# Optimization experiments

Measured on AMD Instinct MI355X. Metric: run time of the kernel, lower is better.

Reference implementation:

```python
import jax, jax.numpy as jnp
import numpy as np


def setup_inputs() -> dict:
    key = jax.random.key(0)
    k1, k2 = jax.random.split(key)
    K, D = 512, 64
    x = jax.random.normal(k1, (64, D, 32, 32), dtype=jnp.float32)
    # torch init: uniform(-1/k, 1/k)
    weight = jax.random.uniform(k2, (D, K), dtype=jnp.float32, minval=-1.0 / K, maxval=1.0 / K)
    return {"x": x, "weight": weight}


def reference(x, weight):
    # x: [B, d, *spatial]; weight: [d, k]
    B, d = x.shape[0], x.shape[1]
    spatial = x.shape[2:]
    xf = x.reshape(B, d, -1)                      # [B, d, N]
    x2 = jnp.sum(xf * xf, axis=1)                 # [B, N]
    w2 = jnp.sum(weight * weight, axis=0)         # [k]
    dots = jnp.einsum('bdn,dk->bnk', xf, weight)  # [B, N, k]
    dist = x2[..., None] - 2.0 * dots + w2        # [B, N, k]
    argmin = jnp.argmin(dist, axis=-1)            # [B, N]
    quantized = jnp.take(weight.T, argmin, axis=0)          # [B, N, d]
    quantized = jnp.moveaxis(quantized.reshape(B, *spatial, d), -1, 1)  # [B, d, *spatial]
    return quantized, argmin.reshape(B, *spatial)
```

## Files before the change

kernel.cpp:

```cpp
#include <hip/hip_runtime.h>

#define KCODES 512
#define DDIM   64
#define NPIX   1024
#define QELEMS (64 * DDIM * NPIX)
#define FLAG_GAP 8e-5f

typedef float f32x4 __attribute__((ext_vector_type(4)));
typedef short bf16x8 __attribute__((ext_vector_type(8)));
typedef unsigned int u32;
typedef u32 u32x4 __attribute__((ext_vector_type(4)));


__device__ __forceinline__ bf16x8 pack_hi(const float* f) {
  u32x4 wds;
#pragma unroll
  for (int p = 0; p < 4; ++p) {
    u32 u0 = __float_as_uint(f[2 * p]);
    u32 u1 = __float_as_uint(f[2 * p + 1]);
    wds[p] = (u0 >> 16) | (u1 & 0xffff0000u);
  }
  return __builtin_bit_cast(bf16x8, wds);
}
__device__ __forceinline__ bf16x8 pack_lo(const float* f) {
  u32x4 wds;
#pragma unroll
  for (int p = 0; p < 4; ++p) {
    float r0 = f[2 * p]     - __uint_as_float(__float_as_uint(f[2 * p])     & 0xffff0000u);
    float r1 = f[2 * p + 1] - __uint_as_float(__float_as_uint(f[2 * p + 1]) & 0xffff0000u);
    wds[p] = (__float_as_uint(r0) >> 16) | (__float_as_uint(r1) & 0xffff0000u);
  }
  return __builtin_bit_cast(bf16x8, wds);
}

__global__ void vq_prep(const float* __restrict__ w,
                        float* __restrict__ w2f_g,
                        bf16x8* __restrict__ frag) {
#pragma clang fp contract(off)
  const int blk = blockIdx.x;
  if (blk == 32) {
    int k = threadIdx.x;
    if (k < KCODES) {
      float s = 0.0f;
      for (int d = 0; d < DDIM; ++d) {
        float v = w[d * KCODES + k];
        float p = v * v;
        s = s + p;
      }
      w2f_g[k] = s;
    }
    return;
  }
  if (threadIdx.x >= 256) return;
  const int cg   = blk;
  const int t    = threadIdx.x >> 6;
  const int lane = threadIdx.x & 63;
  const int code = cg * 16 + (lane & 15);
  const int h    = t & 1;
  float f[8];
#pragma unroll
  for (int j = 0; j < 8; ++j)
    f[j] = w[(h * 32 + (lane >> 4) * 8 + j) * KCODES + code];
  frag[(cg * 4 + t) * 64 + lane] = (t < 2) ? pack_hi(f) : pack_lo(f);
}

__global__ __launch_bounds__(256) void vq_kernel(
    const float* __restrict__ x, const float* __restrict__ w,
    const float* __restrict__ w2f_g, const bf16x8* __restrict__ frag,
    float* __restrict__ qout, float* __restrict__ aout) {
#pragma clang fp contract(off)

  __shared__ float  xs[DDIM][65];
  __shared__ float  sx2[64];
  __shared__ float  w2fs[KCODES];
  __shared__ float  sm1[4][64], sm2[4][64];
  __shared__ int    si1[4][64];
  __shared__ int    skm[64];
  __shared__ unsigned long long s_fmask;

  const int tid  = threadIdx.x;
  const int lane = tid & 63;
  const int lr   = lane & 15;
  const int lg   = lane >> 4;
  const int wid  = __builtin_amdgcn_readfirstlane(tid >> 6);
  const int b    = blockIdx.x >> 4;
  const int n0   = (blockIdx.x & 15) << 6;
  const size_t pixbase = (size_t)blockIdx.x << 6;

  {
    const float* xp = x + (size_t)b * (DDIM * NPIX) + n0;
#pragma unroll
    for (int dd = 0; dd < 16; ++dd) {
      int d = dd * 4 + wid;
      xs[d][lane] = xp[(size_t)d * NPIX + lane];
    }
  }
  w2fs[tid]       = w2f_g[tid];
  w2fs[tid + 256] = w2f_g[tid + 256];
  __syncthreads();

  {
    float x2 = 0.0f;
#pragma unroll
    for (int d = 0; d < DDIM; ++d) {
      float xv = xs[d][lane];
      float p = xv * xv;
      x2 = x2 + p;
    }
    if (tid < 64) sx2[lane] = x2;
  }

  bf16x8 bxh[4][2], bxl[4][2];
#pragma unroll
  for (int pg = 0; pg < 4; ++pg) {
#pragma unroll
    for (int h = 0; h < 2; ++h) {
      float f[8];
#pragma unroll
      for (int j = 0; j < 8; ++j)
        f[j] = xs[h * 32 + lg * 8 + j][pg * 16 + lr];
      bxh[pg][h] = pack_hi(f);
      bxl[pg][h] = pack_lo(f);
    }
  }

  float m1a[4], m2a[4];
  int   i1a[4];
#pragma unroll
  for (int pg = 0; pg < 4; ++pg) { m1a[pg] = 3.4e38f; m2a[pg] = 3.4e38f; i1a[pg] = 0; }

#pragma unroll
  for (int cg = 0; cg < 8; ++cg) {
    const int codebase = wid * 128 + cg * 16;
    const bf16x8* fr = frag + (size_t)(wid * 8 + cg) * 4 * 64 + lane;
    bf16x8 awh0 = fr[0];
    bf16x8 awh1 = fr[64];
    bf16x8 awl0 = fr[128];
    bf16x8 awl1 = fr[192];

#pragma unroll
    for (int pg = 0; pg < 4; ++pg) {
      f32x4 acc = {0.f, 0.f, 0.f, 0.f};
      acc = __builtin_amdgcn_mfma_f32_16x16x32_bf16(awh0, bxh[pg][0], acc, 0, 0, 0);
      acc = __builtin_amdgcn_mfma_f32_16x16x32_bf16(awh1, bxh[pg][1], acc, 0, 0, 0);
      acc = __builtin_amdgcn_mfma_f32_16x16x32_bf16(awl0, bxh[pg][0], acc, 0, 0, 0);
      acc = __builtin_amdgcn_mfma_f32_16x16x32_bf16(awl1, bxh[pg][1], acc, 0, 0, 0);
      acc = __builtin_amdgcn_mfma_f32_16x16x32_bf16(awh0, bxl[pg][0], acc, 0, 0, 0);
      acc = __builtin_amdgcn_mfma_f32_16x16x32_bf16(awh1, bxl[pg][1], acc, 0, 0, 0);
      acc = __builtin_amdgcn_mfma_f32_16x16x32_bf16(awl0, bxl[pg][0], acc, 0, 0, 0);
      acc = __builtin_amdgcn_mfma_f32_16x16x32_bf16(awl1, bxl[pg][1], acc, 0, 0, 0);
#pragma unroll
      for (int r = 0; r < 4; ++r) {
        int code = codebase + lg * 4 + r;
        float s = w2fs[code] - 2.0f * acc[r];
        bool lt = s < m1a[pg];
        float om1 = m1a[pg];
        m2a[pg] = lt ? om1 : fminf(s, m2a[pg]);
        m1a[pg] = lt ? s : m1a[pg];
        i1a[pg] = lt ? code : i1a[pg];
      }
    }
  }

#pragma unroll
  for (int pg = 0; pg < 4; ++pg) {
#pragma unroll
    for (int mi = 0; mi < 2; ++mi) {
      int mask = mi ? 32 : 16;
      float pm1 = __shfl_xor(m1a[pg], mask);
      float pm2 = __shfl_xor(m2a[pg], mask);
      int   pi1 = __shfl_xor(i1a[pg], mask);
      if (pm1 < m1a[pg]) { m2a[pg] = fminf(m1a[pg], pm2); m1a[pg] = pm1; i1a[pg] = pi1; }
      else               { m2a[pg] = fminf(m2a[pg], pm1); }
    }
  }
  if (lg == 0) {
#pragma unroll
    for (int pg = 0; pg < 4; ++pg) {
      sm1[wid][pg * 16 + lr] = m1a[pg];
      sm2[wid][pg * 16 + lr] = m2a[pg];
      si1[wid][pg * 16 + lr] = i1a[pg];
    }
  }
  __syncthreads();

  if (tid < 64) {
    float M1 = sm1[0][lane], M2 = sm2[0][lane];
    int   I1 = si1[0][lane];
#pragma unroll
    for (int c = 1; c < 4; ++c) {
      float c1 = sm1[c][lane];
      if (c1 < M1) { M2 = fminf(M1, sm2[c][lane]); M1 = c1; I1 = si1[c][lane]; }
      else         { M2 = fminf(M2, c1); }
    }
    skm[lane] = I1;
    unsigned long long bal = __ballot(M2 - M1 < FLAG_GAP);
    if (lane == 0) s_fmask = bal;
  }
  __syncthreads();

  {
    unsigned long long fm = s_fmask;
    int idx = 0;
    while (fm) {
      const int L = __builtin_ctzll(fm);
      fm &= (fm - 1);
      if ((idx++ & 3) != wid) continue;
      const float x2L = sx2[L];
      const int k0 = lane * 8;
      float dots[8];
#pragma unroll
      for (int c = 0; c < 8; ++c) dots[c] = 0.f;
      for (int d = 0; d < DDIM; ++d) {
        float xv = xs[d][L];
        const float* wr = w + d * KCODES + k0;
#pragma unroll
        for (int c = 0; c < 8; ++c) {
          float p = xv * wr[c];
          dots[c] = dots[c] + p;
        }
      }
      float bv = 3.4e38f;
      int   bi = 0;
#pragma unroll
      for (int c = 0; c < 8; ++c) {
        float t  = x2L - 2.0f * dots[c];
        float s2 = t + w2fs[k0 + c];
        if (s2 < bv) { bv = s2; bi = k0 + c; }
      }
#pragma unroll
      for (int off = 1; off < 64; off <<= 1) {
        float ov = __shfl_xor(bv, off);
        int   oi = __shfl_xor(bi, off);
        if (ov < bv || (ov == bv && oi < bi)) { bv = ov; bi = oi; }
      }
      if (lane == 0) skm[L] = bi;
    }
  }
  __syncthreads();

  if (tid < 64) aout[pixbase + lane] = (float)skm[lane];

  const int kmin = skm[lane];
  float* qp = qout + (size_t)b * (DDIM * NPIX) + n0 + lane;
#pragma unroll
  for (int dd = 0; dd < 16; ++dd) {
    int d = wid * 16 + dd;
    qp[(size_t)d * NPIX] = w[d * KCODES + kmin];
  }
}

extern "C" void kernel_launch(void* const* d_in, const int* in_sizes, int n_in,
                              void* d_out, int out_size, void* d_ws, size_t ws_size,
                              hipStream_t stream) {
  const float* x = (const float*)d_in[0];
  const float* w = (const float*)d_in[1];
  float* qout = (float*)d_out;
  float* aout = (float*)d_out + QELEMS;

  char*   wsb   = (char*)d_ws;
  float*  w2f_g = (float*)wsb;
  bf16x8* frag  = (bf16x8*)(wsb + 4096);

  vq_prep<<<33, 512, 0, stream>>>(w, w2f_g, frag);
  vq_kernel<<<64 * 16, 256, 0, stream>>>(x, w, w2f_g, frag, qout, aout);
}
```

Baseline: 48.62 us.

## Halve pixels per block, vectorize fp32 fallback loads, tighten flag gap

Each block now handles 32 pixels instead of 64, which doubles the grid to 2048 blocks so more of the GPU is busy. The x tile load and quantized output store are rewritten as flat 256-thread loops over the smaller tile. The exact fp32 recheck loop now reads codebook rows as float4 vectors, unrolled four dimensions at a time. The near-tie threshold that triggers the recheck is halved so fewer pixels take that path. The costs are that each block loads the codebook fragments for half as much work, and a smaller threshold risks missing some near-ties that bf16x3 error could flip.

```diff
diff --git a/kernel.cpp b/kernel.cpp
--- a/kernel.cpp
+++ b/kernel.cpp
@@ -4,7 +4,9 @@
 #define DDIM   64
 #define NPIX   1024
 #define QELEMS (64 * DDIM * NPIX)
-#define FLAG_GAP 8e-5f
+#define PXB    32
+#define NPG    (PXB / 16)
+#define FLAG_GAP 4e-5f
 
 typedef float f32x4 __attribute__((ext_vector_type(4)));
 typedef short bf16x8 __attribute__((ext_vector_type(8)));
@@ -70,12 +72,12 @@
     float* __restrict__ qout, float* __restrict__ aout) {
 #pragma clang fp contract(off)
 
-  __shared__ float  xs[DDIM][65];
-  __shared__ float  sx2[64];
+  __shared__ float  xs[DDIM][PXB + 1];
+  __shared__ float  sx2[PXB];
   __shared__ float  w2fs[KCODES];
-  __shared__ float  sm1[4][64], sm2[4][64];
-  __shared__ int    si1[4][64];
-  __shared__ int    skm[64];
+  __shared__ float  sm1[4][PXB], sm2[4][PXB];
+  __shared__ int    si1[4][PXB];
+  __shared__ int    skm[PXB];
   __shared__ unsigned long long s_fmask;
 
   const int tid  = threadIdx.x;
@@ -83,16 +85,18 @@
   const int lr   = lane & 15;
   const int lg   = lane >> 4;
   const int wid  = __builtin_amdgcn_readfirstlane(tid >> 6);
-  const int b    = blockIdx.x >> 4;
-  const int n0   = (blockIdx.x & 15) << 6;
-  const size_t pixbase = (size_t)blockIdx.x << 6;
+  const int b    = blockIdx.x >> 5;
+  const int n0   = (blockIdx.x & 31) * PXB;
+  const size_t pixbase = (size_t)blockIdx.x * PXB;
 
   {
     const float* xp = x + (size_t)b * (DDIM * NPIX) + n0;
 #pragma unroll
-    for (int dd = 0; dd < 16; ++dd) {
-      int d = dd * 4 + wid;
-      xs[d][lane] = xp[(size_t)d * NPIX + lane];
+    for (int i = 0; i < (DDIM * PXB) / 256; ++i) {
+      int idx = tid + i * 256;
+      int d  = idx >> 5;
+      int px = idx & (PXB - 1);
+      xs[d][px] = xp[(size_t)d * NPIX + px];
     }
   }
   w2fs[tid]       = w2f_g[tid];
@@ -100,19 +104,20 @@
   __syncthreads();
 
   {
+    const int mypx = lane & (PXB - 1);
     float x2 = 0.0f;
 #pragma unroll
     for (int d = 0; d < DDIM; ++d) {
-      float xv = xs[d][lane];
+      float xv = xs[d][mypx];
       float p = xv * xv;
       x2 = x2 + p;
     }
-    if (tid < 64) sx2[lane] = x2;
-  }
-
-  bf16x8 bxh[4][2], bxl[4][2];
-#pragma unroll
-  for (int pg = 0; pg < 4; ++pg) {
+    if (tid < PXB) sx2[tid] = x2;
+  }
+
+  bf16x8 bxh[NPG][2], bxl[NPG][2];
+#pragma unroll
+  for (int pg = 0; pg < NPG; ++pg) {
 #pragma unroll
     for (int h = 0; h < 2; ++h) {
       float f[8];
@@ -124,10 +129,10 @@
     }
   }
 
-  float m1a[4], m2a[4];
-  int   i1a[4];
-#pragma unroll
-  for (int pg = 0; pg < 4; ++pg) { m1a[pg] = 3.4e38f; m2a[pg] = 3.4e38f; i1a[pg] = 0; }
+  float m1a[NPG], m2a[NPG];
+  int   i1a[NPG];
+#pragma unroll
+  for (int pg = 0; pg < NPG; ++pg) { m1a[pg] = 3.4e38f; m2a[pg] = 3.4e38f; i1a[pg] = 0; }
 
 #pragma unroll
   for (int cg = 0; cg < 8; ++cg) {
@@ -139,7 +144,7 @@
     bf16x8 awl1 = fr[192];
 
 #pragma unroll
-    for (int pg = 0; pg < 4; ++pg) {
+    for (int pg = 0; pg < NPG; ++pg) {
       f32x4 acc = {0.f, 0.f, 0.f, 0.f};
       acc = __builtin_amdgcn_mfma_f32_16x16x32_bf16(awh0, bxh[pg][0], acc, 0, 0, 0);
       acc = __builtin_amdgcn_mfma_f32_16x16x32_bf16(awh1, bxh[pg][1], acc, 0, 0, 0);
@@ -163,7 +168,7 @@
   }
 
 #pragma unroll
-  for (int pg = 0; pg < 4; ++pg) {
+  for (int pg = 0; pg < NPG; ++pg) {
 #pragma unroll
     for (int mi = 0; mi < 2; ++mi) {
       int mask = mi ? 32 : 16;
@@ -176,7 +181,7 @@
   }
   if (lg == 0) {
 #pragma unroll
-    for (int pg = 0; pg < 4; ++pg) {
+    for (int pg = 0; pg < NPG; ++pg) {
       sm1[wid][pg * 16 + lr] = m1a[pg];
       sm2[wid][pg * 16 + lr] = m2a[pg];
       si1[wid][pg * 16 + lr] = i1a[pg];
@@ -184,18 +189,18 @@
   }
   __syncthreads();
 
-  if (tid < 64) {
-    float M1 = sm1[0][lane], M2 = sm2[0][lane];
-    int   I1 = si1[0][lane];
+  if (tid < PXB) {
+    float M1 = sm1[0][tid], M2 = sm2[0][tid];
+    int   I1 = si1[0][tid];
 #pragma unroll
     for (int c = 1; c < 4; ++c) {
-      float c1 = sm1[c][lane];
-      if (c1 < M1) { M2 = fminf(M1, sm2[c][lane]); M1 = c1; I1 = si1[c][lane]; }
+      float c1 = sm1[c][tid];
+      if (c1 < M1) { M2 = fminf(M1, sm2[c][tid]); M1 = c1; I1 = si1[c][tid]; }
       else         { M2 = fminf(M2, c1); }
     }
-    skm[lane] = I1;
+    skm[tid] = I1;
     unsigned long long bal = __ballot(M2 - M1 < FLAG_GAP);
-    if (lane == 0) s_fmask = bal;
+    if (tid == 0) s_fmask = bal;
   }
   __syncthreads();
 
@@ -211,13 +216,28 @@
       float dots[8];
 #pragma unroll
       for (int c = 0; c < 8; ++c) dots[c] = 0.f;
-      for (int d = 0; d < DDIM; ++d) {
-        float xv = xs[d][L];
-        const float* wr = w + d * KCODES + k0;
-#pragma unroll
-        for (int c = 0; c < 8; ++c) {
-          float p = xv * wr[c];
-          dots[c] = dots[c] + p;
+      for (int d = 0; d < DDIM; d += 4) {
+        f32x4 wa[4][2];
+        float xv[4];
+#pragma unroll
+        for (int u = 0; u < 4; ++u) {
+          const float* wr = w + (size_t)(d + u) * KCODES + k0;
+          wa[u][0] = *reinterpret_cast<const f32x4*>(wr);
+          wa[u][1] = *reinterpret_cast<const f32x4*>(wr + 4);
+          xv[u] = xs[d + u][L];
+        }
+#pragma unroll
+        for (int u = 0; u < 4; ++u) {
+#pragma unroll
+          for (int c = 0; c < 4; ++c) {
+            float p = xv[u] * wa[u][0][c];
+            dots[c] = dots[c] + p;
+          }
+#pragma unroll
+          for (int c = 0; c < 4; ++c) {
+            float p = xv[u] * wa[u][1][c];
+            dots[c + 4] = dots[c + 4] + p;
+          }
         }
       }
       float bv = 3.4e38f;
@@ -239,14 +259,17 @@
   }
   __syncthreads();
 
-  if (tid < 64) aout[pixbase + lane] = (float)skm[lane];
-
-  const int kmin = skm[lane];
-  float* qp = qout + (size_t)b * (DDIM * NPIX) + n0 + lane;
-#pragma unroll
-  for (int dd = 0; dd < 16; ++dd) {
-    int d = wid * 16 + dd;
-    qp[(size_t)d * NPIX] = w[d * KCODES + kmin];
+  if (tid < PXB) aout[pixbase + tid] = (float)skm[tid];
+
+  {
+    float* qp = qout + (size_t)b * (DDIM * NPIX) + n0;
+#pragma unroll
+    for (int i = 0; i < (DDIM * PXB) / 256; ++i) {
+      int idx = tid + i * 256;
+      int d  = idx >> 5;
+      int px = idx & (PXB - 1);
+      qp[(size_t)d * NPIX + px] = w[d * KCODES + skm[px]];
+    }
   }
 }
 
@@ -263,5 +286,5 @@
   bf16x8* frag  = (bf16x8*)(wsb + 4096);
 
   vq_prep<<<33, 512, 0, stream>>>(w, w2f_g, frag);
-  vq_kernel<<<64 * 16, 256, 0, stream>>>(x, w, w2f_g, frag, qout, aout);
-}
+  vq_kernel<<<(65536 / PXB), 256, 0, stream>>>(x, w, w2f_g, frag, qout, aout);
+}
```

Result: slower. 50.04 us (+2.9%).
